# Kernel optimization log

Measured on AMD Instinct MI355X. Metric: run time of the kernel, lower is better.

## Reference

```python
import jax, jax.numpy as jnp
import numpy as np

B, H, L, DK, DV = 2, 16, 2048, 64, 64


def setup_inputs() -> dict:
    key = jax.random.key(0)
    kq, kk, kv, km = jax.random.split(key, 4)
    return {
        "Q": jax.random.normal(kq, (B, H, L, DK), dtype=jnp.float32),
        "K": jax.random.normal(kk, (B, H, L, DK), dtype=jnp.float32),
        "V": jax.random.normal(kv, (B, H, L, DV), dtype=jnp.float32),
        "attn_mask": jax.random.uniform(km, (L, L), dtype=jnp.float32),
        "d_k": DK,
    }


def reference(Q, K, V, attn_mask, d_k):
    # scores: [B, H, L, L]
    scale = 1.0 / np.sqrt(d_k).astype(np.float32)
    scores = jnp.einsum("bhqd,bhkd->bhqk", Q, K) * scale
    attn = jax.nn.softmax(scores, axis=-1)
    # MSE-style loss vs a 2-D target mask broadcast over (B, H)
    diff = attn - attn_mask[None, None, :, :]
    loss = jnp.sum(diff * diff)
    context = jnp.einsum("bhqk,bhkd->bhqd", attn, V)
    return (context, loss)
```

## Files before the change

### kernel.cpp

```cpp
#include <hip/hip_runtime.h>

#define NHEAD 32
#define LSEQ  2048
#define DIM   64
#define QBLK  64
#define KBLK  64
#define NTILE (LSEQ / KBLK)

typedef float  f32x4  __attribute__((ext_vector_type(4)));
typedef __bf16 bf16x8 __attribute__((ext_vector_type(8)));
typedef unsigned short u16;

__device__ __forceinline__ u16 f2bf(float f) {
    return __builtin_bit_cast(u16, (__bf16)f);
}
__device__ __forceinline__ void st4bf(u16* p, float4 v) {
    union { u16 h[4]; uint2 q; } pk;
    pk.h[0] = f2bf(v.x); pk.h[1] = f2bf(v.y);
    pk.h[2] = f2bf(v.z); pk.h[3] = f2bf(v.w);
    *(uint2*)p = pk.q;
}
__device__ __forceinline__ bf16x8 comb64(const u16* a, const u16* b) {
    union { uint2 q[2]; bf16x8 v; } u;
    u.q[0] = *(const uint2*)a;
    u.q[1] = *(const uint2*)b;
    return u.v;
}

__device__ __forceinline__ void gl_lds16(const u16* g, u16* l) {
    __builtin_amdgcn_global_load_lds(
        (const __attribute__((address_space(1))) void*)g,
        (__attribute__((address_space(3))) void*)l, 16, 0, 0);
}

#define TILE_SYNC() asm volatile("s_waitcnt vmcnt(0)\n\ts_barrier" ::: "memory")

#define QSCALE 0.18033688011112042f
#define RESCALE_THR 8.0f

__global__ void prepack_kernel(const float* __restrict__ K,
                               const float* __restrict__ V,
                               u16* __restrict__ wsK, u16* __restrict__ wsV)
{
    __shared__ float sv[64][65];
    const int b = blockIdx.x;
    const int head = b >> 5, kb = b & 31;
    const int t = threadIdx.x;
    const size_t hoff = (size_t)head * LSEQ * DIM;
    const float* Kg = K + hoff + (size_t)(kb * KBLK) * DIM;
    const float* Vg = V + hoff + (size_t)(kb * KBLK) * DIM;
    u16* outK = wsK + (size_t)b * 4096;
    u16* outV = wsV + (size_t)b * 4096;

#pragma unroll
    for (int i = 0; i < 16; ++i) {
        const int e = t + 256 * i;
        sv[e >> 6][e & 63] = Vg[e];
    }
#pragma unroll
    for (int i = 0; i < 2; ++i) {
        const int c = t + 256 * i;
        const int r = c >> 3, q = c & 7;
        const int d0 = 8 * (q ^ (r & 7));
        float4 a  = *(const float4*)(Kg + r * DIM + d0);
        float4 bb = *(const float4*)(Kg + r * DIM + d0 + 4);
        union { u16 h[8]; uint4 u; } pk;
        pk.h[0]=f2bf(a.x);  pk.h[1]=f2bf(a.y);  pk.h[2]=f2bf(a.z);  pk.h[3]=f2bf(a.w);
        pk.h[4]=f2bf(bb.x); pk.h[5]=f2bf(bb.y); pk.h[6]=f2bf(bb.z); pk.h[7]=f2bf(bb.w);
        *(uint4*)(outK + c * 8) = pk.u;
    }
    __syncthreads();
#pragma unroll
    for (int i = 0; i < 2; ++i) {
        const int c = t + 256 * i;
        const int d = c >> 3, q = c & 7;
        const int cl = q ^ (d & 7);
        const int mp = cl >> 2, lq = cl & 3;
        union { u16 h[8]; uint4 u; } pk;
#pragma unroll
        for (int s = 0; s < 2; ++s) {
            const int k0 = 4 * (8 * mp + 4 * s + lq);
#pragma unroll
            for (int j = 0; j < 4; ++j)
                pk.h[4 * s + j] = f2bf(sv[k0 + j][d]);
        }
        *(uint4*)(outV + c * 8) = pk.u;
    }
}

__launch_bounds__(256, 4)
__global__ void attn_fused_kernel(const float* __restrict__ Q,
                                  const u16* __restrict__ wsK,
                                  const u16* __restrict__ wsV,
                                  const float* __restrict__ Msk,
                                  float* __restrict__ out,
                                  float* __restrict__ loss)
{
    __shared__ __align__(16) u16 lds_k[2][4096];
    __shared__ __align__(16) u16 lds_v[2][4096];

    const int t  = threadIdx.x;
    const int wg   = ((int)blockIdx.x & 7) * 128 + ((int)blockIdx.x >> 3);
    const int head = wg >> 5;
    const int qb   = wg & 31;
    const int qbase = qb * QBLK;
    const int w  = t >> 6;
    const int l  = t & 63;
    const int lr = l & 15;
    const int lq = l >> 4;
    const int x7 = lr & 7;

    const size_t hoff = (size_t)head * LSEQ * DIM;
    const int qg = qbase + 16 * w + lr;

    bf16x8 qf[2];
#pragma unroll
    for (int s = 0; s < 2; ++s) {
        const float* src = Q + hoff + (size_t)qg * DIM + 32 * s + 8 * lq;
        float4 a = *(const float4*)(src);
        float4 b = *(const float4*)(src + 4);
        union { u16 h[8]; bf16x8 v; } u;
        u.h[0] = f2bf(a.x * QSCALE); u.h[1] = f2bf(a.y * QSCALE);
        u.h[2] = f2bf(a.z * QSCALE); u.h[3] = f2bf(a.w * QSCALE);
        u.h[4] = f2bf(b.x * QSCALE); u.h[5] = f2bf(b.y * QSCALE);
        u.h[6] = f2bf(b.z * QSCALE); u.h[7] = f2bf(b.w * QSCALE);
        qf[s] = u.v;
    }

    f32x4 acc[4];
#pragma unroll
    for (int dt = 0; dt < 4; ++dt) acc[dt] = (f32x4){0.f, 0.f, 0.f, 0.f};
    float mrun = -1e30f, lrun = 0.f, la2 = 0.f, lam = 0.f;

    const u16* srcK = wsK + (size_t)(head * NTILE) * 4096 + t * 8;
    const u16* srcV = wsV + (size_t)(head * NTILE) * 4096 + t * 8;

    auto stage = [&](int buf, int kb) {
        const u16* gk = srcK + (size_t)kb * 4096;
        const u16* gv = srcV + (size_t)kb * 4096;
        gl_lds16(gk,        &lds_k[buf][t * 8]);
        gl_lds16(gk + 2048, &lds_k[buf][t * 8 + 2048]);
        gl_lds16(gv,        &lds_v[buf][t * 8]);
        gl_lds16(gv + 2048, &lds_v[buf][t * 8 + 2048]);
    };

    stage(0, 0);
    int cur = 0;

    for (int kb = 0; kb < NTILE; ++kb) {
        TILE_SYNC();

        f32x4 mreg[4];
        {
            const float* mp_ = Msk + (size_t)qg * LSEQ + kb * KBLK + 4 * lq;
#pragma unroll
            for (int m = 0; m < 4; ++m)
                mreg[m] = *(const f32x4*)(mp_ + 16 * m);
        }

        if (kb + 1 < NTILE) stage(cur ^ 1, kb + 1);

        f32x4 S[4];
        __builtin_amdgcn_s_setprio(1);
#pragma unroll
        for (int m = 0; m < 4; ++m) {
            const u16* kro = &lds_k[cur][(16 * m + lr) * 64];
            bf16x8 kf0 = *(const bf16x8*)(kro + ((lq ^ x7) << 3));
            bf16x8 kf1 = *(const bf16x8*)(kro + (((lq + 4) ^ x7) << 3));
            f32x4 z = (f32x4){0.f, 0.f, 0.f, 0.f};
            z = __builtin_amdgcn_mfma_f32_16x16x32_bf16(kf0, qf[0], z, 0, 0, 0);
            z = __builtin_amdgcn_mfma_f32_16x16x32_bf16(kf1, qf[1], z, 0, 0, 0);
            S[m] = z;
        }
        __builtin_amdgcn_s_setprio(0);

        float tm = fmaxf(fmaxf(fmaxf(S[0][0], S[0][1]), fmaxf(S[0][2], S[0][3])),
                         fmaxf(fmaxf(S[1][0], S[1][1]), fmaxf(S[1][2], S[1][3])));
        tm = fmaxf(tm, fmaxf(fmaxf(fmaxf(S[2][0], S[2][1]), fmaxf(S[2][2], S[2][3])),
                             fmaxf(fmaxf(S[3][0], S[3][1]), fmaxf(S[3][2], S[3][3]))));
        tm = fmaxf(tm, __shfl_xor(tm, 16));
        tm = fmaxf(tm, __shfl_xor(tm, 32));
        if (!__all(tm - mrun <= RESCALE_THR)) {
            const float mn = fmaxf(mrun, tm);
            const float al = __builtin_amdgcn_exp2f(mrun - mn);
            mrun = mn;
            lrun *= al; la2 *= al * al; lam *= al;
#pragma unroll
            for (int dt = 0; dt < 4; ++dt) acc[dt] *= al;
        }

        float psum = 0.f, pp2 = 0.f, ppm = 0.f;
        u16 pb[16];
#pragma unroll
        for (int m = 0; m < 4; ++m) {
#pragma unroll
            for (int r = 0; r < 4; ++r) {
                float p = __builtin_amdgcn_exp2f(S[m][r] - mrun);
                psum += p;
                pp2  += p * p;
                ppm  += p * mreg[m][r];
                pb[4 * m + r] = f2bf(p);
            }
        }
        lrun += psum; la2 += pp2; lam += ppm;

        bf16x8 pf[2];
#pragma unroll
        for (int mp = 0; mp < 2; ++mp) {
            union { u16 h[8]; bf16x8 v; } u;
#pragma unroll
            for (int j = 0; j < 4; ++j) { u.h[j] = pb[8 * mp + j]; u.h[4 + j] = pb[8 * mp + 4 + j]; }
            pf[mp] = u.v;
        }
        __builtin_amdgcn_s_setprio(1);
#pragma unroll
        for (int dt = 0; dt < 4; ++dt) {
            const u16* vro = &lds_v[cur][(16 * dt + lr) * 64];
#pragma unroll
            for (int mp = 0; mp < 2; ++mp) {
                bf16x8 vf = *(const bf16x8*)(vro + (((4 * mp + lq) ^ x7) << 3));
                acc[dt] = __builtin_amdgcn_mfma_f32_16x16x32_bf16(vf, pf[mp], acc[dt], 0, 0, 0);
            }
        }
        __builtin_amdgcn_s_setprio(0);
        cur ^= 1;
    }

#pragma unroll
    for (int off = 16; off <= 32; off <<= 1) {
        lrun += __shfl_xor(lrun, off);
        la2  += __shfl_xor(la2,  off);
        lam  += __shfl_xor(lam,  off);
    }

    const float inv = 1.0f / lrun;

#pragma unroll
    for (int dt = 0; dt < 4; ++dt) {
        float4 o;
        o.x = acc[dt][0] * inv; o.y = acc[dt][1] * inv;
        o.z = acc[dt][2] * inv; o.w = acc[dt][3] * inv;
        *(float4*)(out + hoff + (size_t)qg * DIM + 16 * dt + 4 * lq) = o;
    }

    float part = la2 * inv * inv - 2.0f * lam * inv;
    part = (l < 16) ? part : 0.f;
#pragma unroll
    for (int off = 1; off <= 8; off <<= 1) part += __shfl_xor(part, off);
    if (l == 0) atomicAdd(loss, part);
}

__launch_bounds__(256, 4)
__global__ void attn_fallback_kernel(const float* __restrict__ Q,
                                     const float* __restrict__ K,
                                     const float* __restrict__ V,
                                     const float* __restrict__ Msk,
                                     float* __restrict__ out,
                                     float* __restrict__ loss)
{
    __shared__ __align__(16) u16 lds_k[64][72];
    __shared__ __align__(16) u16 lds_v[64][68];

    const int t  = threadIdx.x;
    const int wg   = ((int)blockIdx.x & 7) * 128 + ((int)blockIdx.x >> 3);
    const int head = wg >> 5;
    const int qb   = wg & 31;
    const int qbase = qb * QBLK;
    const int w  = t >> 6;
    const int l  = t & 63;
    const int lr = l & 15;
    const int lq = l >> 4;

    const size_t hoff = (size_t)head * LSEQ * DIM;
    const int qg = qbase + 16 * w + lr;

    bf16x8 qf[2];
#pragma unroll
    for (int s = 0; s < 2; ++s) {
        const float* src = Q + hoff + (size_t)qg * DIM + 32 * s + 8 * lq;
        float4 a = *(const float4*)(src);
        float4 b = *(const float4*)(src + 4);
        union { u16 h[8]; bf16x8 v; } u;
        u.h[0] = f2bf(a.x * QSCALE); u.h[1] = f2bf(a.y * QSCALE);
        u.h[2] = f2bf(a.z * QSCALE); u.h[3] = f2bf(a.w * QSCALE);
        u.h[4] = f2bf(b.x * QSCALE); u.h[5] = f2bf(b.y * QSCALE);
        u.h[6] = f2bf(b.z * QSCALE); u.h[7] = f2bf(b.w * QSCALE);
        qf[s] = u.v;
    }

    f32x4 acc[4];
#pragma unroll
    for (int dt = 0; dt < 4; ++dt) acc[dt] = (f32x4){0.f, 0.f, 0.f, 0.f};
    float mrun = -1e30f, lrun = 0.f, la2 = 0.f, lam = 0.f;

    for (int kb = 0; kb < NTILE; ++kb) {
        const int kbase = kb * KBLK;
        __syncthreads();
        f32x4 mreg[4];
        {
            const float* mp_ = Msk + (size_t)qg * LSEQ + kbase + 4 * lq;
#pragma unroll
            for (int m = 0; m < 4; ++m)
                mreg[m] = *(const f32x4*)(mp_ + 16 * m);
        }
        {
            const float* Kg = K + hoff + (size_t)kbase * DIM;
            const float* Vg = V + hoff + (size_t)kbase * DIM;
#pragma unroll
            for (int i = 0; i < 4; ++i) {
                const int id = t + 256 * i;
                const int r = id >> 4, c = (id & 15) * 4;
                float4 kv = *(const float4*)(Kg + r * DIM + c);
                float4 vv = *(const float4*)(Vg + r * DIM + c);
                st4bf(&lds_k[r][c], kv);
                lds_v[c + 0][r] = f2bf(vv.x);
                lds_v[c + 1][r] = f2bf(vv.y);
                lds_v[c + 2][r] = f2bf(vv.z);
                lds_v[c + 3][r] = f2bf(vv.w);
            }
        }
        __syncthreads();

        f32x4 S[4];
#pragma unroll
        for (int m = 0; m < 4; ++m) {
            bf16x8 kf0 = *(const bf16x8*)&lds_k[16 * m + lr][8 * lq];
            bf16x8 kf1 = *(const bf16x8*)&lds_k[16 * m + lr][32 + 8 * lq];
            f32x4 z = (f32x4){0.f, 0.f, 0.f, 0.f};
            z = __builtin_amdgcn_mfma_f32_16x16x32_bf16(kf0, qf[0], z, 0, 0, 0);
            z = __builtin_amdgcn_mfma_f32_16x16x32_bf16(kf1, qf[1], z, 0, 0, 0);
            S[m] = z;
        }

        float tm = fmaxf(fmaxf(fmaxf(S[0][0], S[0][1]), fmaxf(S[0][2], S[0][3])),
                         fmaxf(fmaxf(S[1][0], S[1][1]), fmaxf(S[1][2], S[1][3])));
        tm = fmaxf(tm, fmaxf(fmaxf(fmaxf(S[2][0], S[2][1]), fmaxf(S[2][2], S[2][3])),
                             fmaxf(fmaxf(S[3][0], S[3][1]), fmaxf(S[3][2], S[3][3]))));
        tm = fmaxf(tm, __shfl_xor(tm, 16));
        tm = fmaxf(tm, __shfl_xor(tm, 32));
        if (!__all(tm - mrun <= RESCALE_THR)) {
            const float mn = fmaxf(mrun, tm);
            const float al = __builtin_amdgcn_exp2f(mrun - mn);
            mrun = mn;
            lrun *= al; la2 *= al * al; lam *= al;
#pragma unroll
            for (int dt = 0; dt < 4; ++dt) acc[dt] *= al;
        }

        float psum = 0.f, pp2 = 0.f, ppm = 0.f;
        u16 pb[16];
#pragma unroll
        for (int m = 0; m < 4; ++m) {
#pragma unroll
            for (int r = 0; r < 4; ++r) {
                float p = __builtin_amdgcn_exp2f(S[m][r] - mrun);
                psum += p;
                pp2  += p * p;
                ppm  += p * mreg[m][r];
                pb[4 * m + r] = f2bf(p);
            }
        }
        lrun += psum; la2 += pp2; lam += ppm;

        bf16x8 pf[2];
#pragma unroll
        for (int mp = 0; mp < 2; ++mp) {
            union { u16 h[8]; bf16x8 v; } u;
#pragma unroll
            for (int j = 0; j < 4; ++j) { u.h[j] = pb[8 * mp + j]; u.h[4 + j] = pb[8 * mp + 4 + j]; }
            pf[mp] = u.v;
        }
#pragma unroll
        for (int dt = 0; dt < 4; ++dt) {
#pragma unroll
            for (int mp = 0; mp < 2; ++mp) {
                bf16x8 vf = comb64(&lds_v[16 * dt + lr][32 * mp + 4 * lq],
                                   &lds_v[16 * dt + lr][32 * mp + 16 + 4 * lq]);
                acc[dt] = __builtin_amdgcn_mfma_f32_16x16x32_bf16(vf, pf[mp], acc[dt], 0, 0, 0);
            }
        }
    }

#pragma unroll
    for (int off = 16; off <= 32; off <<= 1) {
        lrun += __shfl_xor(lrun, off);
        la2  += __shfl_xor(la2,  off);
        lam  += __shfl_xor(lam,  off);
    }
    const float inv = 1.0f / lrun;
#pragma unroll
    for (int dt = 0; dt < 4; ++dt) {
        float4 o;
        o.x = acc[dt][0] * inv; o.y = acc[dt][1] * inv;
        o.z = acc[dt][2] * inv; o.w = acc[dt][3] * inv;
        *(float4*)(out + hoff + (size_t)qg * DIM + 16 * dt + 4 * lq) = o;
    }
    float part = la2 * inv * inv - 2.0f * lam * inv;
    part = (l < 16) ? part : 0.f;
#pragma unroll
    for (int off = 1; off <= 8; off <<= 1) part += __shfl_xor(part, off);
    if (l == 0) atomicAdd(loss, part);
}

__global__ void masksq_kernel(const float* __restrict__ Msk, float* __restrict__ loss)
{
    __shared__ float red[4];
    float s = 0.f;
    const size_t n4 = (size_t)LSEQ * LSEQ / 4;
    for (size_t i = (size_t)blockIdx.x * blockDim.x + threadIdx.x; i < n4;
         i += (size_t)gridDim.x * blockDim.x) {
        float4 v = ((const float4*)Msk)[i];
        s += v.x * v.x + v.y * v.y + v.z * v.z + v.w * v.w;
    }
#pragma unroll
    for (int off = 1; off <= 32; off <<= 1) s += __shfl_xor(s, off);
    if ((threadIdx.x & 63) == 0) red[threadIdx.x >> 6] = s;
    __syncthreads();
    if (threadIdx.x == 0) {
        float tot = red[0] + red[1] + red[2] + red[3];
        atomicAdd(loss, 32.0f * tot);
    }
}

extern "C" void kernel_launch(void* const* d_in, const int* in_sizes, int n_in,
                              void* d_out, int out_size, void* d_ws, size_t ws_size,
                              hipStream_t stream)
{
    const float* Q   = (const float*)d_in[0];
    const float* K   = (const float*)d_in[1];
    const float* V   = (const float*)d_in[2];
    const float* Msk = (const float*)d_in[3];
    float* out  = (float*)d_out;
    float* loss = out + (size_t)NHEAD * LSEQ * DIM;

    hipMemsetAsync(loss, 0, sizeof(float), stream);
    masksq_kernel<<<256, 256, 0, stream>>>(Msk, loss);

    const size_t need = (size_t)2 * NHEAD * NTILE * 4096 * sizeof(u16);
    if (d_ws && ws_size >= need) {
        u16* wsK = (u16*)d_ws;
        u16* wsV = wsK + (size_t)NHEAD * NTILE * 4096;
        prepack_kernel<<<NHEAD * NTILE, 256, 0, stream>>>(K, V, wsK, wsV);
        attn_fused_kernel<<<NHEAD * (LSEQ / QBLK), 256, 0, stream>>>(Q, wsK, wsV, Msk, out, loss);
    } else {
        attn_fallback_kernel<<<NHEAD * (LSEQ / QBLK), 256, 0, stream>>>(Q, K, V, Msk, out, loss);
    }
}
```

Before: 147.1 us.

## Fuse mask-square sum into prepack and unroll attention loop by two with prefetch

The separate mask-squared reduction kernel is folded into the prepack kernel, so each prepack block also reduces one 4096-float slice of the mask, which removes a kernel launch. The attention main loop is manually unrolled by two with fixed LDS buffers, and the next tile's mask values are prefetched into registers one iteration ahead. V fragments are now loaded before the softmax so their LDS latency overlaps the exp work. The cross-lane max shuffle is moved inside the rescale branch. This raises register pressure through the double mask buffers and eight held V fragments. The shuffle move also means the rescale test now uses each lane's own local maximum rather than the row-wide one.

```diff
diff --git a/kernel.cpp b/kernel.cpp
--- a/kernel.cpp
+++ b/kernel.cpp
@@ -40,9 +40,12 @@
 
 __global__ void prepack_kernel(const float* __restrict__ K,
                                const float* __restrict__ V,
-                               u16* __restrict__ wsK, u16* __restrict__ wsV)
+                               const float* __restrict__ Msk,
+                               u16* __restrict__ wsK, u16* __restrict__ wsV,
+                               float* __restrict__ loss)
 {
     __shared__ float sv[64][65];
+    __shared__ float red2[4];
     const int b = blockIdx.x;
     const int head = b >> 5, kb = b & 31;
     const int t = threadIdx.x;
@@ -86,6 +89,20 @@
         }
         *(uint4*)(outV + c * 8) = pk.u;
     }
+
+    float s = 0.f;
+    const float4* mq = (const float4*)(Msk + (size_t)b * 4096);
+#pragma unroll
+    for (int i = 0; i < 4; ++i) {
+        float4 v = mq[t + 256 * i];
+        s += v.x * v.x + v.y * v.y + v.z * v.z + v.w * v.w;
+    }
+#pragma unroll
+    for (int off = 1; off <= 32; off <<= 1) s += __shfl_xor(s, off);
+    if ((t & 63) == 0) red2[t >> 6] = s;
+    __syncthreads();
+    if (t == 0)
+        atomicAdd(loss, 32.0f * (red2[0] + red2[1] + red2[2] + red2[3]));
 }
 
 __launch_bounds__(256, 4)
@@ -144,27 +161,20 @@
         gl_lds16(gv + 2048, &lds_v[buf][t * 8 + 2048]);
     };
 
-    stage(0, 0);
-    int cur = 0;
-
-    for (int kb = 0; kb < NTILE; ++kb) {
-        TILE_SYNC();
-
-        f32x4 mreg[4];
-        {
-            const float* mp_ = Msk + (size_t)qg * LSEQ + kb * KBLK + 4 * lq;
-#pragma unroll
-            for (int m = 0; m < 4; ++m)
-                mreg[m] = *(const f32x4*)(mp_ + 16 * m);
-        }
-
-        if (kb + 1 < NTILE) stage(cur ^ 1, kb + 1);
-
+    f32x4 mA[4], mB[4];
+    auto ldmask = [&](int kb, f32x4* d) {
+        const float* mp_ = Msk + (size_t)qg * LSEQ + kb * KBLK + 4 * lq;
+#pragma unroll
+        for (int m = 0; m < 4; ++m)
+            d[m] = *(const f32x4*)(mp_ + 16 * m);
+    };
+
+    auto body = [&](const u16* bk, const u16* bv, const f32x4* mreg) {
         f32x4 S[4];
         __builtin_amdgcn_s_setprio(1);
 #pragma unroll
         for (int m = 0; m < 4; ++m) {
-            const u16* kro = &lds_k[cur][(16 * m + lr) * 64];
+            const u16* kro = bk + (16 * m + lr) * 64;
             bf16x8 kf0 = *(const bf16x8*)(kro + ((lq ^ x7) << 3));
             bf16x8 kf1 = *(const bf16x8*)(kro + (((lq + 4) ^ x7) << 3));
             f32x4 z = (f32x4){0.f, 0.f, 0.f, 0.f};
@@ -173,6 +183,202 @@
             S[m] = z;
         }
         __builtin_amdgcn_s_setprio(0);
+
+        bf16x8 vf[8];
+#pragma unroll
+        for (int dt = 0; dt < 4; ++dt)
+#pragma unroll
+            for (int mp = 0; mp < 2; ++mp)
+                vf[2 * dt + mp] =
+                    *(const bf16x8*)(bv + (16 * dt + lr) * 64 + (((4 * mp + lq) ^ x7) << 3));
+
+        float tm = fmaxf(fmaxf(fmaxf(S[0][0], S[0][1]), fmaxf(S[0][2], S[0][3])),
+                         fmaxf(fmaxf(S[1][0], S[1][1]), fmaxf(S[1][2], S[1][3])));
+        tm = fmaxf(tm, fmaxf(fmaxf(fmaxf(S[2][0], S[2][1]), fmaxf(S[2][2], S[2][3])),
+                             fmaxf(fmaxf(S[3][0], S[3][1]), fmaxf(S[3][2], S[3][3]))));
+        if (!__all(tm - mrun <= RESCALE_THR)) {
+            tm = fmaxf(tm, __shfl_xor(tm, 16));
+            tm = fmaxf(tm, __shfl_xor(tm, 32));
+            const float mn = fmaxf(mrun, tm);
+            const float al = __builtin_amdgcn_exp2f(mrun - mn);
+            mrun = mn;
+            lrun *= al; la2 *= al * al; lam *= al;
+#pragma unroll
+            for (int dt = 0; dt < 4; ++dt) acc[dt] *= al;
+        }
+
+        float psum = 0.f, pp2 = 0.f, ppm = 0.f;
+        u16 pb[16];
+#pragma unroll
+        for (int m = 0; m < 4; ++m) {
+#pragma unroll
+            for (int r = 0; r < 4; ++r) {
+                float p = __builtin_amdgcn_exp2f(S[m][r] - mrun);
+                psum += p;
+                pp2  += p * p;
+                ppm  += p * mreg[m][r];
+                pb[4 * m + r] = f2bf(p);
+            }
+        }
+        lrun += psum; la2 += pp2; lam += ppm;
+
+        bf16x8 pf[2];
+#pragma unroll
+        for (int mp = 0; mp < 2; ++mp) {
+            union { u16 h[8]; bf16x8 v; } u;
+#pragma unroll
+            for (int j = 0; j < 4; ++j) { u.h[j] = pb[8 * mp + j]; u.h[4 + j] = pb[8 * mp + 4 + j]; }
+            pf[mp] = u.v;
+        }
+        __builtin_amdgcn_s_setprio(1);
+#pragma unroll
+        for (int dt = 0; dt < 4; ++dt)
+#pragma unroll
+            for (int mp = 0; mp < 2; ++mp)
+                acc[dt] = __builtin_amdgcn_mfma_f32_16x16x32_bf16(vf[2 * dt + mp], pf[mp],
+                                                                  acc[dt], 0, 0, 0);
+        __builtin_amdgcn_s_setprio(0);
+    };
+
+    stage(0, 0);
+    ldmask(0, mA);
+
+    for (int kb = 0; kb < NTILE; kb += 2) {
+        TILE_SYNC();
+        stage(1, kb + 1);
+        ldmask(kb + 1, mB);
+        body(lds_k[0], lds_v[0], mA);
+
+        TILE_SYNC();
+        if (kb + 2 < NTILE) { stage(0, kb + 2); ldmask(kb + 2, mA); }
+        body(lds_k[1], lds_v[1], mB);
+    }
+
+#pragma unroll
+    for (int off = 16; off <= 32; off <<= 1) {
+        lrun += __shfl_xor(lrun, off);
+        la2  += __shfl_xor(la2,  off);
+        lam  += __shfl_xor(lam,  off);
+    }
+
+    const float inv = 1.0f / lrun;
+
+#pragma unroll
+    for (int dt = 0; dt < 4; ++dt) {
+        float4 o;
+        o.x = acc[dt][0] * inv; o.y = acc[dt][1] * inv;
+        o.z = acc[dt][2] * inv; o.w = acc[dt][3] * inv;
+        *(float4*)(out + hoff + (size_t)qg * DIM + 16 * dt + 4 * lq) = o;
+    }
+
+    float part = la2 * inv * inv - 2.0f * lam * inv;
+    part = (l < 16) ? part : 0.f;
+#pragma unroll
+    for (int off = 1; off <= 8; off <<= 1) part += __shfl_xor(part, off);
+    if (l == 0) atomicAdd(loss, part);
+}
+
+__global__ void masksq_kernel(const float* __restrict__ Msk, float* __restrict__ loss)
+{
+    __shared__ float red[4];
+    float s = 0.f;
+    const size_t n4 = (size_t)LSEQ * LSEQ / 4;
+    for (size_t i = (size_t)blockIdx.x * blockDim.x + threadIdx.x; i < n4;
+         i += (size_t)gridDim.x * blockDim.x) {
+        float4 v = ((const float4*)Msk)[i];
+        s += v.x * v.x + v.y * v.y + v.z * v.z + v.w * v.w;
+    }
+#pragma unroll
+    for (int off = 1; off <= 32; off <<= 1) s += __shfl_xor(s, off);
+    if ((threadIdx.x & 63) == 0) red[threadIdx.x >> 6] = s;
+    __syncthreads();
+    if (threadIdx.x == 0) {
+        float tot = red[0] + red[1] + red[2] + red[3];
+        atomicAdd(loss, 32.0f * tot);
+    }
+}
+
+__launch_bounds__(256, 4)
+__global__ void attn_fallback_kernel(const float* __restrict__ Q,
+                                     const float* __restrict__ K,
+                                     const float* __restrict__ V,
+                                     const float* __restrict__ Msk,
+                                     float* __restrict__ out,
+                                     float* __restrict__ loss)
+{
+    __shared__ __align__(16) u16 lds_k[64][72];
+    __shared__ __align__(16) u16 lds_v[64][68];
+
+    const int t  = threadIdx.x;
+    const int wg   = ((int)blockIdx.x & 7) * 128 + ((int)blockIdx.x >> 3);
+    const int head = wg >> 5;
+    const int qb   = wg & 31;
+    const int qbase = qb * QBLK;
+    const int w  = t >> 6;
+    const int l  = t & 63;
+    const int lr = l & 15;
+    const int lq = l >> 4;
+
+    const size_t hoff = (size_t)head * LSEQ * DIM;
+    const int qg = qbase + 16 * w + lr;
+
+    bf16x8 qf[2];
+#pragma unroll
+    for (int s = 0; s < 2; ++s) {
+        const float* src = Q + hoff + (size_t)qg * DIM + 32 * s + 8 * lq;
+        float4 a = *(const float4*)(src);
+        float4 b = *(const float4*)(src + 4);
+        union { u16 h[8]; bf16x8 v; } u;
+        u.h[0] = f2bf(a.x * QSCALE); u.h[1] = f2bf(a.y * QSCALE);
+        u.h[2] = f2bf(a.z * QSCALE); u.h[3] = f2bf(a.w * QSCALE);
+        u.h[4] = f2bf(b.x * QSCALE); u.h[5] = f2bf(b.y * QSCALE);
+        u.h[6] = f2bf(b.z * QSCALE); u.h[7] = f2bf(b.w * QSCALE);
+        qf[s] = u.v;
+    }
+
+    f32x4 acc[4];
+#pragma unroll
+    for (int dt = 0; dt < 4; ++dt) acc[dt] = (f32x4){0.f, 0.f, 0.f, 0.f};
+    float mrun = -1e30f, lrun = 0.f, la2 = 0.f, lam = 0.f;
+
+    for (int kb = 0; kb < NTILE; ++kb) {
+        const int kbase = kb * KBLK;
+        __syncthreads();
+        f32x4 mreg[4];
+        {
+            const float* mp_ = Msk + (size_t)qg * LSEQ + kbase + 4 * lq;
+#pragma unroll
+            for (int m = 0; m < 4; ++m)
+                mreg[m] = *(const f32x4*)(mp_ + 16 * m);
+        }
+        {
+            const float* Kg = K + hoff + (size_t)kbase * DIM;
+            const float* Vg = V + hoff + (size_t)kbase * DIM;
+#pragma unroll
+            for (int i = 0; i < 4; ++i) {
+                const int id = t + 256 * i;
+                const int r = id >> 4, c = (id & 15) * 4;
+                float4 kv = *(const float4*)(Kg + r * DIM + c);
+                float4 vv = *(const float4*)(Vg + r * DIM + c);
+                st4bf(&lds_k[r][c], kv);
+                lds_v[c + 0][r] = f2bf(vv.x);
+                lds_v[c + 1][r] = f2bf(vv.y);
+                lds_v[c + 2][r] = f2bf(vv.z);
+                lds_v[c + 3][r] = f2bf(vv.w);
+            }
+        }
+        __syncthreads();
+
+        f32x4 S[4];
+#pragma unroll
+        for (int m = 0; m < 4; ++m) {
+            bf16x8 kf0 = *(const bf16x8*)&lds_k[16 * m + lr][8 * lq];
+            bf16x8 kf1 = *(const bf16x8*)&lds_k[16 * m + lr][32 + 8 * lq];
+            f32x4 z = (f32x4){0.f, 0.f, 0.f, 0.f};
+            z = __builtin_amdgcn_mfma_f32_16x16x32_bf16(kf0, qf[0], z, 0, 0, 0);
+            z = __builtin_amdgcn_mfma_f32_16x16x32_bf16(kf1, qf[1], z, 0, 0, 0);
+            S[m] = z;
+        }
 
         float tm = fmaxf(fmaxf(fmaxf(S[0][0], S[0][1]), fmaxf(S[0][2], S[0][3])),
                          fmaxf(fmaxf(S[1][0], S[1][1]), fmaxf(S[1][2], S[1][3])));
@@ -212,18 +418,15 @@
             for (int j = 0; j < 4; ++j) { u.h[j] = pb[8 * mp + j]; u.h[4 + j] = pb[8 * mp + 4 + j]; }
             pf[mp] = u.v;
         }
-        __builtin_amdgcn_s_setprio(1);
 #pragma unroll
         for (int dt = 0; dt < 4; ++dt) {
-            const u16* vro = &lds_v[cur][(16 * dt + lr) * 64];
 #pragma unroll
             for (int mp = 0; mp < 2; ++mp) {
-                bf16x8 vf = *(const bf16x8*)(vro + (((4 * mp + lq) ^ x7) << 3));
+                bf16x8 vf = comb64(&lds_v[16 * dt + lr][32 * mp + 4 * lq],
+                                   &lds_v[16 * dt + lr][32 * mp + 16 + 4 * lq]);
                 acc[dt] = __builtin_amdgcn_mfma_f32_16x16x32_bf16(vf, pf[mp], acc[dt], 0, 0, 0);
             }
         }
-        __builtin_amdgcn_s_setprio(0);
-        cur ^= 1;
     }
 
 #pragma unroll
@@ -232,9 +435,7 @@
         la2  += __shfl_xor(la2,  off);
         lam  += __shfl_xor(lam,  off);
     }
-
     const float inv = 1.0f / lrun;
-
 #pragma unroll
     for (int dt = 0; dt < 4; ++dt) {
         float4 o;
@@ -242,184 +443,11 @@
         o.z = acc[dt][2] * inv; o.w = acc[dt][3] * inv;
         *(float4*)(out + hoff + (size_t)qg * DIM + 16 * dt + 4 * lq) = o;
     }
-
     float part = la2 * inv * inv - 2.0f * lam * inv;
     part = (l < 16) ? part : 0.f;
 #pragma unroll
     for (int off = 1; off <= 8; off <<= 1) part += __shfl_xor(part, off);
     if (l == 0) atomicAdd(loss, part);
-}
-
-__launch_bounds__(256, 4)
-__global__ void attn_fallback_kernel(const float* __restrict__ Q,
-                                     const float* __restrict__ K,
-                                     const float* __restrict__ V,
-                                     const float* __restrict__ Msk,
-                                     float* __restrict__ out,
-                                     float* __restrict__ loss)
-{
-    __shared__ __align__(16) u16 lds_k[64][72];
-    __shared__ __align__(16) u16 lds_v[64][68];
-
-    const int t  = threadIdx.x;
-    const int wg   = ((int)blockIdx.x & 7) * 128 + ((int)blockIdx.x >> 3);
-    const int head = wg >> 5;
-    const int qb   = wg & 31;
-    const int qbase = qb * QBLK;
-    const int w  = t >> 6;
-    const int l  = t & 63;
-    const int lr = l & 15;
-    const int lq = l >> 4;
-
-    const size_t hoff = (size_t)head * LSEQ * DIM;
-    const int qg = qbase + 16 * w + lr;
-
-    bf16x8 qf[2];
-#pragma unroll
-    for (int s = 0; s < 2; ++s) {
-        const float* src = Q + hoff + (size_t)qg * DIM + 32 * s + 8 * lq;
-        float4 a = *(const float4*)(src);
-        float4 b = *(const float4*)(src + 4);
-        union { u16 h[8]; bf16x8 v; } u;
-        u.h[0] = f2bf(a.x * QSCALE); u.h[1] = f2bf(a.y * QSCALE);
-        u.h[2] = f2bf(a.z * QSCALE); u.h[3] = f2bf(a.w * QSCALE);
-        u.h[4] = f2bf(b.x * QSCALE); u.h[5] = f2bf(b.y * QSCALE);
-        u.h[6] = f2bf(b.z * QSCALE); u.h[7] = f2bf(b.w * QSCALE);
-        qf[s] = u.v;
-    }
-
-    f32x4 acc[4];
-#pragma unroll
-    for (int dt = 0; dt < 4; ++dt) acc[dt] = (f32x4){0.f, 0.f, 0.f, 0.f};
-    float mrun = -1e30f, lrun = 0.f, la2 = 0.f, lam = 0.f;
-
-    for (int kb = 0; kb < NTILE; ++kb) {
-        const int kbase = kb * KBLK;
-        __syncthreads();
-        f32x4 mreg[4];
-        {
-            const float* mp_ = Msk + (size_t)qg * LSEQ + kbase + 4 * lq;
-#pragma unroll
-            for (int m = 0; m < 4; ++m)
-                mreg[m] = *(const f32x4*)(mp_ + 16 * m);
-        }
-        {
-            const float* Kg = K + hoff + (size_t)kbase * DIM;
-            const float* Vg = V + hoff + (size_t)kbase * DIM;
-#pragma unroll
-            for (int i = 0; i < 4; ++i) {
-                const int id = t + 256 * i;
-                const int r = id >> 4, c = (id & 15) * 4;
-                float4 kv = *(const float4*)(Kg + r * DIM + c);
-                float4 vv = *(const float4*)(Vg + r * DIM + c);
-                st4bf(&lds_k[r][c], kv);
-                lds_v[c + 0][r] = f2bf(vv.x);
-                lds_v[c + 1][r] = f2bf(vv.y);
-                lds_v[c + 2][r] = f2bf(vv.z);
-                lds_v[c + 3][r] = f2bf(vv.w);
-            }
-        }
-        __syncthreads();
-
-        f32x4 S[4];
-#pragma unroll
-        for (int m = 0; m < 4; ++m) {
-            bf16x8 kf0 = *(const bf16x8*)&lds_k[16 * m + lr][8 * lq];
-            bf16x8 kf1 = *(const bf16x8*)&lds_k[16 * m + lr][32 + 8 * lq];
-            f32x4 z = (f32x4){0.f, 0.f, 0.f, 0.f};
-            z = __builtin_amdgcn_mfma_f32_16x16x32_bf16(kf0, qf[0], z, 0, 0, 0);
-            z = __builtin_amdgcn_mfma_f32_16x16x32_bf16(kf1, qf[1], z, 0, 0, 0);
-            S[m] = z;
-        }
-
-        float tm = fmaxf(fmaxf(fmaxf(S[0][0], S[0][1]), fmaxf(S[0][2], S[0][3])),
-                         fmaxf(fmaxf(S[1][0], S[1][1]), fmaxf(S[1][2], S[1][3])));
-        tm = fmaxf(tm, fmaxf(fmaxf(fmaxf(S[2][0], S[2][1]), fmaxf(S[2][2], S[2][3])),
-                             fmaxf(fmaxf(S[3][0], S[3][1]), fmaxf(S[3][2], S[3][3]))));
-        tm = fmaxf(tm, __shfl_xor(tm, 16));
-        tm = fmaxf(tm, __shfl_xor(tm, 32));
-        if (!__all(tm - mrun <= RESCALE_THR)) {
-            const float mn = fmaxf(mrun, tm);
-            const float al = __builtin_amdgcn_exp2f(mrun - mn);
-            mrun = mn;
-            lrun *= al; la2 *= al * al; lam *= al;
-#pragma unroll
-            for (int dt = 0; dt < 4; ++dt) acc[dt] *= al;
-        }
-
-        float psum = 0.f, pp2 = 0.f, ppm = 0.f;
-        u16 pb[16];
-#pragma unroll
-        for (int m = 0; m < 4; ++m) {
-#pragma unroll
-            for (int r = 0; r < 4; ++r) {
-                float p = __builtin_amdgcn_exp2f(S[m][r] - mrun);
-                psum += p;
-                pp2  += p * p;
-                ppm  += p * mreg[m][r];
-                pb[4 * m + r] = f2bf(p);
-            }
-        }
-        lrun += psum; la2 += pp2; lam += ppm;
-
-        bf16x8 pf[2];
-#pragma unroll
-        for (int mp = 0; mp < 2; ++mp) {
-            union { u16 h[8]; bf16x8 v; } u;
-#pragma unroll
-            for (int j = 0; j < 4; ++j) { u.h[j] = pb[8 * mp + j]; u.h[4 + j] = pb[8 * mp + 4 + j]; }
-            pf[mp] = u.v;
-        }
-#pragma unroll
-        for (int dt = 0; dt < 4; ++dt) {
-#pragma unroll
-            for (int mp = 0; mp < 2; ++mp) {
-                bf16x8 vf = comb64(&lds_v[16 * dt + lr][32 * mp + 4 * lq],
-                                   &lds_v[16 * dt + lr][32 * mp + 16 + 4 * lq]);
-                acc[dt] = __builtin_amdgcn_mfma_f32_16x16x32_bf16(vf, pf[mp], acc[dt], 0, 0, 0);
-            }
-        }
-    }
-
-#pragma unroll
-    for (int off = 16; off <= 32; off <<= 1) {
-        lrun += __shfl_xor(lrun, off);
-        la2  += __shfl_xor(la2,  off);
-        lam  += __shfl_xor(lam,  off);
-    }
-    const float inv = 1.0f / lrun;
-#pragma unroll
-    for (int dt = 0; dt < 4; ++dt) {
-        float4 o;
-        o.x = acc[dt][0] * inv; o.y = acc[dt][1] * inv;
-        o.z = acc[dt][2] * inv; o.w = acc[dt][3] * inv;
-        *(float4*)(out + hoff + (size_t)qg * DIM + 16 * dt + 4 * lq) = o;
-    }
-    float part = la2 * inv * inv - 2.0f * lam * inv;
-    part = (l < 16) ? part : 0.f;
-#pragma unroll
-    for (int off = 1; off <= 8; off <<= 1) part += __shfl_xor(part, off);
-    if (l == 0) atomicAdd(loss, part);
-}
-
-__global__ void masksq_kernel(const float* __restrict__ Msk, float* __restrict__ loss)
-{
-    __shared__ float red[4];
-    float s = 0.f;
-    const size_t n4 = (size_t)LSEQ * LSEQ / 4;
-    for (size_t i = (size_t)blockIdx.x * blockDim.x + threadIdx.x; i < n4;
-         i += (size_t)gridDim.x * blockDim.x) {
-        float4 v = ((const float4*)Msk)[i];
-        s += v.x * v.x + v.y * v.y + v.z * v.z + v.w * v.w;
-    }
-#pragma unroll
-    for (int off = 1; off <= 32; off <<= 1) s += __shfl_xor(s, off);
-    if ((threadIdx.x & 63) == 0) red[threadIdx.x >> 6] = s;
-    __syncthreads();
-    if (threadIdx.x == 0) {
-        float tot = red[0] + red[1] + red[2] + red[3];
-        atomicAdd(loss, 32.0f * tot);
-    }
 }
 
 extern "C" void kernel_launch(void* const* d_in, const int* in_sizes, int n_in,
@@ -434,15 +462,15 @@
     float* loss = out + (size_t)NHEAD * LSEQ * DIM;
 
     hipMemsetAsync(loss, 0, sizeof(float), stream);
-    masksq_kernel<<<256, 256, 0, stream>>>(Msk, loss);
 
     const size_t need = (size_t)2 * NHEAD * NTILE * 4096 * sizeof(u16);
     if (d_ws && ws_size >= need) {
         u16* wsK = (u16*)d_ws;
         u16* wsV = wsK + (size_t)NHEAD * NTILE * 4096;
-        prepack_kernel<<<NHEAD * NTILE, 256, 0, stream>>>(K, V, wsK, wsV);
+        prepack_kernel<<<NHEAD * NTILE, 256, 0, stream>>>(K, V, Msk, wsK, wsV, loss);
         attn_fused_kernel<<<NHEAD * (LSEQ / QBLK), 256, 0, stream>>>(Q, wsK, wsV, Msk, out, loss);
     } else {
+        masksq_kernel<<<256, 256, 0, stream>>>(Msk, loss);
         attn_fallback_kernel<<<NHEAD * (LSEQ / QBLK), 256, 0, stream>>>(Q, K, V, Msk, out, loss);
     }
 }
```

Result: slower. 185.0 us (+25.7%).
